# Optimization experiments

Hardware: AMD Instinct MI355X
Metric: run time of the kernel (lower is better)

## Reference

```python
import jax, jax.numpy as jnp
import numpy as np

N = 100000
E = 50000
NNZ = 300000
F_IN = 128
F_OUT = 128


def setup_inputs() -> dict:
    key = jax.random.key(0)
    ks = jax.random.split(key, 10)
    X = jax.random.normal(ks[0], (N, F_IN), dtype=jnp.float32)
    X0 = jax.random.normal(ks[1], (N, F_IN), dtype=jnp.float32)
    vertex = jax.random.randint(ks[2], (NNZ,), 0, N, dtype=jnp.int32)
    edges = jax.random.randint(ks[3], (NNZ,), 0, E, dtype=jnp.int32)
    # params init per reset_parameters: uniform(0.02, 0.05)
    u = lambda k, s: jax.random.uniform(k, s, jnp.float32, 0.02, 0.05)
    w_b = u(ks[4], (2 * F_IN, F_OUT))
    w_a = u(ks[5], (2 * F_IN, F_OUT))
    w_c = u(ks[6], (2 * F_IN, F_OUT))
    b_b = u(ks[7], (1, F_OUT))
    b_a = u(ks[8], (1, F_OUT))
    b_c = u(ks[9], (1, F_OUT))
    return {"X": X, "vertex": vertex, "edges": edges, "X0": X0,
            "n_edges": E, "w_b": w_b, "w_a": w_a, "w_c": w_c,
            "b_b": b_b, "b_a": b_a, "b_c": b_c}


def reference(X, vertex, edges, X0, n_edges, w_b, w_a, w_c, b_b, b_a, b_c):
    n = X.shape[-2]
    # round 1: node -> hyperedge aggregation (scatter-add by edge id)
    Xve = X[vertex]                                        # [nnz, F]
    Xe = jax.ops.segment_sum(Xve, edges, num_segments=n_edges)  # [E, F]
    # round 2: hyperedge -> node, concat with gathered node features
    Xev = jnp.concatenate([X[vertex], Xe[edges]], axis=-1)  # [nnz, 2F]
    Xv = jax.ops.segment_sum(Xev, vertex, num_segments=n)   # [N, 2F]
    # normalization is Identity (InputNorm=False)
    center = Xv @ w_b + b_b                 # [N, F_OUT]
    aXv = jnp.abs(Xv)
    scope_l = aXv @ w_a + b_a
    scope_r = aXv @ w_c + b_c
    HL = center - scope_l
    HR = center + scope_r
    return (center, HL, HR)
```

## Files before the change

### kernel.cpp

```cpp
#include <hip/hip_runtime.h>
#include <cstddef>
#include <cstdint>

#define F 128
#define E_FIXED 50000
#define SCAN_ELEMS 2048

typedef __attribute__((ext_vector_type(8))) short short8;
typedef __attribute__((ext_vector_type(4))) float f32x4;
typedef __attribute__((ext_vector_type(4))) unsigned int uint32x4;
typedef __attribute__((address_space(3))) unsigned int lds_uint;
typedef const __attribute__((address_space(1))) unsigned int glb_uint;

__device__ inline unsigned short f32_to_bf16(float f) {
  union { float f; unsigned int u; } v; v.f = f;
  unsigned int u = v.u;
  unsigned int r = u + 0x7FFFu + ((u >> 16) & 1u);
  return (unsigned short)(r >> 16);
}

__global__ __launch_bounds__(256) void init_kernel(
    int* __restrict__ zp, int n4, int zb,
    const float* __restrict__ wb, const float* __restrict__ wa,
    const float* __restrict__ wc, unsigned short* __restrict__ wt) {
  int b = blockIdx.x;
  int t = threadIdx.x;
  if (b < zb) {
    int i = b * 256 + t;
    if (i < n4) reinterpret_cast<int4*>(zp)[i] = make_int4(0, 0, 0, 0);
    return;
  }
  int id = (b - zb) * 256 + t;
  int mat = id >> 15;
  int r = id & 32767;
  int k = r >> 7;
  int col = r & 127;
  int ks = k >> 5;
  int kg = (k >> 3) & 3;
  int e  = k & 7;
  int ct = col >> 4;
  int bc = col & 15;
  int lane = kg * 16 + bc;
  const float* w = (mat == 0) ? wb : ((mat == 1) ? wa : wc);
  size_t off = ((((size_t)(ks * 3 + mat) * 8 + ct) * 64 + lane) * 8 + e);
  wt[off] = f32_to_bf16(w[r]);
}

__global__ __launch_bounds__(256) void count_kernel(
    const int* __restrict__ vertex, const int* __restrict__ edges,
    int* __restrict__ cnt, int nnz, int E) {
  int i = blockIdx.x * 256 + threadIdx.x;
  if (i >= nnz) return;
  atomicAdd(cnt + edges[i], 1);
  atomicAdd(cnt + E + vertex[i], 1);
}

__global__ __launch_bounds__(256) void scan_lookback_kernel(
    const int* __restrict__ cnt, int* __restrict__ off,
    int* __restrict__ state, int L) {
  __shared__ int s[256];
  __shared__ int sprefix;
  const int b = blockIdx.x;
  const int t = threadIdx.x;
  const int base = b * SCAN_ELEMS + t * 8;
  int v[8];
  if (base + 8 <= L) {
    int4 a0 = *reinterpret_cast<const int4*>(cnt + base);
    int4 a1 = *reinterpret_cast<const int4*>(cnt + base + 4);
    v[0] = a0.x; v[1] = a0.y; v[2] = a0.z; v[3] = a0.w;
    v[4] = a1.x; v[5] = a1.y; v[6] = a1.z; v[7] = a1.w;
  } else {
    #pragma unroll
    for (int j = 0; j < 8; ++j) v[j] = (base + j < L) ? cnt[base + j] : 0;
  }
  int tsum = 0;
  #pragma unroll
  for (int j = 0; j < 8; ++j) tsum += v[j];
  s[t] = tsum;
  __syncthreads();
  #pragma unroll
  for (int d = 1; d < 256; d <<= 1) {
    int val = (t >= d) ? s[t - d] : 0;
    __syncthreads();
    s[t] += val;
    __syncthreads();
  }
  if (t == 0) {
    int bsum = s[255];
    __hip_atomic_store(&state[128 + b], bsum, __ATOMIC_RELAXED, __HIP_MEMORY_SCOPE_AGENT);
    __hip_atomic_store(&state[b], 1, __ATOMIC_RELEASE, __HIP_MEMORY_SCOPE_AGENT);
    int prefix = 0;
    for (int j = b - 1; j >= 0; --j) {
      int f;
      do {
        f = __hip_atomic_load(&state[j], __ATOMIC_ACQUIRE, __HIP_MEMORY_SCOPE_AGENT);
      } while (f == 0);
      if (f == 2) {
        prefix += __hip_atomic_load(&state[256 + j], __ATOMIC_RELAXED, __HIP_MEMORY_SCOPE_AGENT);
        break;
      }
      prefix += __hip_atomic_load(&state[128 + j], __ATOMIC_RELAXED, __HIP_MEMORY_SCOPE_AGENT);
    }
    __hip_atomic_store(&state[256 + b], prefix + bsum, __ATOMIC_RELAXED, __HIP_MEMORY_SCOPE_AGENT);
    __hip_atomic_store(&state[b], 2, __ATOMIC_RELEASE, __HIP_MEMORY_SCOPE_AGENT);
    sprefix = prefix;
  }
  __syncthreads();
  int run = sprefix + (s[t] - tsum);
  #pragma unroll
  for (int j = 0; j < 8; ++j) {
    int idx = base + j;
    if (idx < L) off[idx] = run;
    run += v[j];
  }
}

__global__ __launch_bounds__(256) void fill_kernel(
    const int* __restrict__ vertex, const int* __restrict__ edges,
    const int* __restrict__ off, int* __restrict__ cur,
    int* __restrict__ csr, int nnz, int E) {
  int i = blockIdx.x * 256 + threadIdx.x;
  if (i >= nnz) return;
  int v = vertex[i], e = edges[i];
  int p = atomicAdd(cur + e, 1);
  csr[off[e] + p] = v;
  int q = atomicAdd(cur + E + v, 1);
  csr[off[E + v] + q] = e;
}

__global__ __launch_bounds__(256) void gather_edge_kernel(
    const float* __restrict__ X, const int* __restrict__ off,
    const int* __restrict__ cnt, const int* __restrict__ csr,
    unsigned short* __restrict__ Xe_b, int E) {
  int gid = blockIdx.x * 256 + threadIdx.x;
  int e = gid >> 6;
  int lane = threadIdx.x & 63;
  if (e >= E) return;
  int start = off[e], n = cnt[e];
  float2 acc = make_float2(0.f, 0.f);
  for (int j = 0; j < n; ++j) {
    int v = csr[start + j];
    float2 x = *reinterpret_cast<const float2*>(X + (size_t)v * F + lane * 2);
    acc.x += x.x; acc.y += x.y;
  }
  unsigned int pk = (unsigned int)f32_to_bf16(acc.x) |
                    ((unsigned int)f32_to_bf16(acc.y) << 16);
  *reinterpret_cast<unsigned int*>(Xe_b + (size_t)e * F + lane * 2) = pk;
}

__global__ __launch_bounds__(256) void gather_vertex_kernel(
    const unsigned short* __restrict__ Xe_b, const int* __restrict__ off,
    const int* __restrict__ cnt, const int* __restrict__ csr,
    unsigned short* __restrict__ Xv2_b, int E, int N) {
  int gid = blockIdx.x * 256 + threadIdx.x;
  int v = gid >> 6;
  int lane = threadIdx.x & 63;
  if (v >= N) return;
  int start = off[E + v], n = cnt[E + v];
  float2 acc = make_float2(0.f, 0.f);
  for (int j = 0; j < n; ++j) {
    int e = csr[start + j];
    unsigned int u = *reinterpret_cast<const unsigned int*>(
        Xe_b + (size_t)e * F + lane * 2);
    union { unsigned int u; float f; } lo, hi;
    lo.u = u << 16; hi.u = u & 0xFFFF0000u;
    acc.x += lo.f; acc.y += hi.f;
  }
  unsigned int pk = (unsigned int)f32_to_bf16(acc.x) |
                    ((unsigned int)f32_to_bf16(acc.y) << 16);
  *reinterpret_cast<unsigned int*>(Xv2_b + (size_t)v * F + lane * 2) = pk;
}

__global__ __launch_bounds__(512, 4) void fused_mfma_kernel(
    const float* __restrict__ X,
    const unsigned short* __restrict__ Xv2_b,
    const int* __restrict__ deg,
    const unsigned short* __restrict__ wt,
    const float* __restrict__ bb, const float* __restrict__ ba,
    const float* __restrict__ bc,
    float* __restrict__ out, int N) {
  __shared__ unsigned short wlds[48 * 512];
  const int t = threadIdx.x;
  const int wave = t >> 6;
  const int lane = t & 63;
  const int node0 = blockIdx.x * 128;
  const int node = node0 + wave * 16 + (lane & 15);
  const int kg = lane >> 4;

  uint32x4 a[8];
  const bool ok = node < N;
  const float dg = ok ? (float)deg[node] : 0.f;
  #pragma unroll
  for (int ks = 0; ks < 4; ++ks) {
    float4 f0 = make_float4(0.f, 0.f, 0.f, 0.f);
    float4 f1 = make_float4(0.f, 0.f, 0.f, 0.f);
    if (ok) {
      const float* src = X + (size_t)node * F + ks * 32 + kg * 8;
      f0 = *reinterpret_cast<const float4*>(src);
      f1 = *reinterpret_cast<const float4*>(src + 4);
      f0.x *= dg; f0.y *= dg; f0.z *= dg; f0.w *= dg;
      f1.x *= dg; f1.y *= dg; f1.z *= dg; f1.w *= dg;
    }
    uint32x4 p;
    p[0] = (unsigned int)f32_to_bf16(f0.x) | ((unsigned int)f32_to_bf16(f0.y) << 16);
    p[1] = (unsigned int)f32_to_bf16(f0.z) | ((unsigned int)f32_to_bf16(f0.w) << 16);
    p[2] = (unsigned int)f32_to_bf16(f1.x) | ((unsigned int)f32_to_bf16(f1.y) << 16);
    p[3] = (unsigned int)f32_to_bf16(f1.z) | ((unsigned int)f32_to_bf16(f1.w) << 16);
    a[ks] = p;
  }
  #pragma unroll
  for (int ks = 4; ks < 8; ++ks) {
    uint32x4 p = (uint32x4)(0u);
    if (ok)
      p = *reinterpret_cast<const uint32x4*>(
          Xv2_b + (size_t)node * F + (ks - 4) * 32 + kg * 8);
    a[ks] = p;
  }

  const int nrow0 = node0 + wave * 16 + (lane >> 4) * 4;

  #pragma unroll
  for (int h = 0; h < 4; ++h) {
    #pragma unroll
    for (int i = 0; i < 3; ++i) {
      int p = wave * 3 + i;
      #pragma unroll
      for (int c = 0; c < 2; ++c) {
        int g = p * 8 + h * 2 + c;
        int q = p * 2 + c;
        __builtin_amdgcn_global_load_lds(
            (glb_uint*)(wt + (size_t)g * 512 + lane * 8),
            (lds_uint*)(&wlds[q * 512]), 16, 0, 0);
      }
    }
    __syncthreads();

    f32x4 acc[3][2];
    #pragma unroll
    for (int m = 0; m < 3; ++m)
      #pragma unroll
      for (int c = 0; c < 2; ++c) acc[m][c] = (f32x4)(0.f);

    #pragma unroll
    for (int ks = 0; ks < 8; ++ks) {
      uint32x4 av = a[ks];
      uint32x4 aav = av & 0x7FFF7FFFu;
      short8 A  = __builtin_bit_cast(short8, av);
      short8 AA = __builtin_bit_cast(short8, aav);
      #pragma unroll
      for (int m = 0; m < 3; ++m) {
        short8 Ause = (m == 0) ? A : AA;
        #pragma unroll
        for (int c = 0; c < 2; ++c) {
          int q = (ks * 3 + m) * 2 + c;
          short8 B = *reinterpret_cast<const short8*>(&wlds[q * 512 + lane * 8]);
          acc[m][c] = __builtin_amdgcn_mfma_f32_16x16x32_bf16(Ause, B, acc[m][c], 0, 0, 0);
        }
      }
    }

    #pragma unroll
    for (int c = 0; c < 2; ++c) {
      int col = h * 32 + c * 16 + (lane & 15);
      float vb = bb[col], va = ba[col], vc = bc[col];
      #pragma unroll
      for (int j = 0; j < 4; ++j) {
        int nd = nrow0 + j;
        if (nd < N) {
          float ce = acc[0][c][j] + vb;
          float sl = acc[1][c][j] + va;
          float sr = acc[2][c][j] + vc;
          out[(size_t)nd * F + col] = ce;
          out[((size_t)N + nd) * F + col] = ce - sl;
          out[((size_t)2 * N + nd) * F + col] = ce + sr;
        }
      }
    }
    __syncthreads();
  }
}

extern "C" void kernel_launch(void* const* d_in, const int* in_sizes, int n_in,
                              void* d_out, int out_size, void* d_ws, size_t ws_size,
                              hipStream_t stream) {
  const float* X      = (const float*)d_in[0];
  const int*   vertex = (const int*)d_in[1];
  const int*   edges  = (const int*)d_in[2];
  const float* wb = (const float*)d_in[5];
  const float* wa = (const float*)d_in[6];
  const float* wc = (const float*)d_in[7];
  const float* bb = (const float*)d_in[8];
  const float* ba = (const float*)d_in[9];
  const float* bc = (const float*)d_in[10];

  const int N   = in_sizes[0] / F;
  const int nnz = in_sizes[1];
  const int E   = E_FIXED;
  const int L   = E + N;
  const int nb  = (L + SCAN_ELEMS - 1) / SCAN_ELEMS;

  unsigned short* Xe_b  = (unsigned short*)d_ws;
  unsigned short* Xv2_b = Xe_b + (size_t)E * F;
  unsigned short* wt    = Xv2_b + (size_t)N * F;
  int* cnt   = (int*)(wt + 3 * 32768);
  int* cur   = cnt + L;
  int* state = cur + L;
  int* off   = state + 384;
  int* csr   = off + L;

  int n4 = (2 * L + 384) / 4;
  int zb = (n4 + 255) / 256;
  init_kernel<<<zb + 384, 256, 0, stream>>>(cnt, n4, zb, wb, wa, wc, wt);

  int blocks_nnz = (nnz + 255) / 256;
  count_kernel<<<blocks_nnz, 256, 0, stream>>>(vertex, edges, cnt, nnz, E);

  scan_lookback_kernel<<<nb, 256, 0, stream>>>(cnt, off, state, L);

  fill_kernel<<<blocks_nnz, 256, 0, stream>>>(vertex, edges, off, cur, csr, nnz, E);

  gather_edge_kernel<<<(E * 64 + 255) / 256, 256, 0, stream>>>(
      X, off, cnt, csr, Xe_b, E);
  gather_vertex_kernel<<<(N * 64 + 255) / 256, 256, 0, stream>>>(
      Xe_b, off, cnt, csr, Xv2_b, E, N);

  int blocks_g = (N + 127) / 128;
  fused_mfma_kernel<<<blocks_g, 512, 0, stream>>>(
      X, Xv2_b, cnt + E, wt, bb, ba, bc, (float*)d_out, N);
}
```

Before: 218.5 us.

## Double-buffer weight tiles in LDS and prefetch next column slice during MFMA

```diff
diff --git a/kernel.cpp b/kernel.cpp
--- a/kernel.cpp
+++ b/kernel.cpp
@@ -179,13 +179,21 @@
     const float* __restrict__ bb, const float* __restrict__ ba,
     const float* __restrict__ bc,
     float* __restrict__ out, int N) {
-  __shared__ unsigned short wlds[48 * 512];
+  __shared__ unsigned short wlds[2][24 * 512];
   const int t = threadIdx.x;
   const int wave = t >> 6;
   const int lane = t & 63;
   const int node0 = blockIdx.x * 128;
   const int node = node0 + wave * 16 + (lane & 15);
   const int kg = lane >> 4;
+
+  #pragma unroll
+  for (int i = 0; i < 3; ++i) {
+    int f = wave * 3 + i;
+    __builtin_amdgcn_global_load_lds(
+        (glb_uint*)(wt + ((size_t)f * 8 + 0) * 512 + lane * 8),
+        (lds_uint*)(&wlds[0][f * 512]), 16, 0, 0);
+  }
 
   uint32x4 a[8];
   const bool ok = node < N;
@@ -216,30 +224,26 @@
           Xv2_b + (size_t)node * F + (ks - 4) * 32 + kg * 8);
     a[ks] = p;
   }
+  __syncthreads();
 
   const int nrow0 = node0 + wave * 16 + (lane >> 4) * 4;
 
   #pragma unroll
-  for (int h = 0; h < 4; ++h) {
+  for (int p = 0; p < 8; ++p) {
+    const int cur = p & 1;
+    if (p < 7) {
+      #pragma unroll
+      for (int i = 0; i < 3; ++i) {
+        int f = wave * 3 + i;
+        __builtin_amdgcn_global_load_lds(
+            (glb_uint*)(wt + ((size_t)f * 8 + (p + 1)) * 512 + lane * 8),
+            (lds_uint*)(&wlds[cur ^ 1][f * 512]), 16, 0, 0);
+      }
+    }
+
+    f32x4 acc[3];
     #pragma unroll
-    for (int i = 0; i < 3; ++i) {
-      int p = wave * 3 + i;
-      #pragma unroll
-      for (int c = 0; c < 2; ++c) {
-        int g = p * 8 + h * 2 + c;
-        int q = p * 2 + c;
-        __builtin_amdgcn_global_load_lds(
-            (glb_uint*)(wt + (size_t)g * 512 + lane * 8),
-            (lds_uint*)(&wlds[q * 512]), 16, 0, 0);
-      }
-    }
-    __syncthreads();
-
-    f32x4 acc[3][2];
-    #pragma unroll
-    for (int m = 0; m < 3; ++m)
-      #pragma unroll
-      for (int c = 0; c < 2; ++c) acc[m][c] = (f32x4)(0.f);
+    for (int m = 0; m < 3; ++m) acc[m] = (f32x4)(0.f);
 
     #pragma unroll
     for (int ks = 0; ks < 8; ++ks) {
@@ -250,26 +254,22 @@
       #pragma unroll
       for (int m = 0; m < 3; ++m) {
         short8 Ause = (m == 0) ? A : AA;
-        #pragma unroll
-        for (int c = 0; c < 2; ++c) {
-          int q = (ks * 3 + m) * 2 + c;
-          short8 B = *reinterpret_cast<const short8*>(&wlds[q * 512 + lane * 8]);
-          acc[m][c] = __builtin_amdgcn_mfma_f32_16x16x32_bf16(Ause, B, acc[m][c], 0, 0, 0);
-        }
+        short8 B = *reinterpret_cast<const short8*>(
+            &wlds[cur][(ks * 3 + m) * 512 + lane * 8]);
+        acc[m] = __builtin_amdgcn_mfma_f32_16x16x32_bf16(Ause, B, acc[m], 0, 0, 0);
       }
     }
 
-    #pragma unroll
-    for (int c = 0; c < 2; ++c) {
-      int col = h * 32 + c * 16 + (lane & 15);
+    {
+      int col = p * 16 + (lane & 15);
       float vb = bb[col], va = ba[col], vc = bc[col];
       #pragma unroll
       for (int j = 0; j < 4; ++j) {
         int nd = nrow0 + j;
         if (nd < N) {
-          float ce = acc[0][c][j] + vb;
-          float sl = acc[1][c][j] + va;
-          float sr = acc[2][c][j] + vc;
+          float ce = acc[0][j] + vb;
+          float sl = acc[1][j] + va;
+          float sr = acc[2][j] + vc;
           out[(size_t)nd * F + col] = ce;
           out[((size_t)N + nd) * F + col] = ce - sl;
           out[((size_t)2 * N + nd) * F + col] = ce + sr;
```

Result: no change. 221.4 us (+1.3%).
